# Optimization experiments

Hardware: AMD Instinct MI355X
Metric: run time of the kernel (lower is better)

Reference implementation:

```python
import jax, jax.numpy as jnp
import numpy as np

SCALE = 0.2
ASPECT = 1.0
ORIGIN = (0.5, 0.5)
AREA_THRESH = 400


def setup_inputs() -> dict:
    key = jax.random.key(0)
    kb, ki, kp, kd = jax.random.split(key, 4)
    B, N, H, W = 16, 16, 640, 640
    k1, k2, k3, k4 = jax.random.split(kb, 4)
    ymin = jax.random.uniform(k1, (B, N)) * 280.0
    xmin = jax.random.uniform(k2, (B, N)) * 280.0
    h = 150.0 + jax.random.uniform(k3, (B, N)) * 170.0
    w = 150.0 + jax.random.uniform(k4, (B, N)) * 170.0
    boxes = jnp.stack([ymin, xmin, h, w], axis=-1)  # [B,N,4] = [ymin,xmin,h,w]
    images = jax.random.uniform(ki, (B, H, W, 3), dtype=jnp.float32)
    patch = jax.random.uniform(kp, (300, 300, 3), dtype=jnp.float32)
    transform_decisions = jax.random.bernoulli(kd, 0.5, (B, N, 3))  # rot90, flip_lr, flip_ud
    return {"boxes": boxes, "images": images, "patch": patch,
            "transform_decisions": transform_decisions}


def _bilinear_sample(patch, sy, sx):
    # tf.image.resize (v2 bilinear, half-pixel centers) expressed as a gather.
    Hp, Wp, _ = patch.shape
    sy = jnp.clip(sy, 0.0, Hp - 1.0)
    sx = jnp.clip(sx, 0.0, Wp - 1.0)
    y0 = jnp.floor(sy).astype(jnp.int32)
    x0 = jnp.floor(sx).astype(jnp.int32)
    y1 = jnp.minimum(y0 + 1, Hp - 1)
    x1 = jnp.minimum(x0 + 1, Wp - 1)
    wy = (sy - y0)[..., None]
    wx = (sx - x0)[..., None]
    p00 = patch[y0, x0]; p01 = patch[y0, x1]
    p10 = patch[y1, x0]; p11 = patch[y1, x1]
    top = p00 * (1.0 - wx) + p01 * wx
    bot = p10 * (1.0 - wx) + p11 * wx
    return top * (1.0 - wy) + bot * wy  # [H,W,C]


def _patch_boxes(boxes, H, W):
    # Patcher.create(): place a scale*h square patch at box origin, clamp to image.
    ymin, xmin, h, w = (boxes[..., i] for i in range(4))
    ph = h * SCALE
    pw = ASPECT * ph
    y0 = ymin + h * ORIGIN[1]
    x0 = xmin + w * ORIGIN[0]
    y0 = jnp.where(y0 + ph > H, H - ph, y0)
    x0 = jnp.where(x0 + pw > W, W - pw, x0)
    return jnp.stack([y0, x0, ph, pw], axis=-1)


def _forward(boxes, images, patch, transform_decisions):
    B, H, W, C = images.shape
    Hp, Wp, _ = patch.shape
    pboxes = _patch_boxes(boxes, float(H), float(W))  # [B,N,4] float
    bi = pboxes.astype(jnp.int32)                     # tf.cast truncation
    valid = (bi[..., 2] * bi[..., 3]) > AREA_THRESH   # area filter (mask, not ragged)
    Y = jnp.arange(H)[:, None]
    X = jnp.arange(W)[None, :]

    def apply_patch(img, carry):
        box, dec, v = carry
        y0i, x0i = box[0], box[1]
        s = jnp.maximum(box[2], 1)  # square side (aspect=1); guard div-by-zero
        iy = Y - y0i                 # local patch coords of every image pixel
        ix = X - x0i
        inside = (iy >= 0) & (iy < s) & (ix >= 0) & (ix < s) & v
        iyc = jnp.clip(iy, 0, s - 1)
        ixc = jnp.clip(ix, 0, s - 1)
        d0, d1, d2 = dec[0], dec[1], dec[2]
        iy2 = jnp.where(d2, s - 1 - iyc, iyc)  # invert flip_up_down
        ix2 = jnp.where(d1, s - 1 - ixc, ixc)  # invert flip_left_right
        ry = jnp.where(d0, ix2, iy2)           # invert rot90 (CCW): out[i,j]=in[j,s-1-i]
        rx = jnp.where(d0, s - 1 - iy2, ix2)
        sf = s.astype(jnp.float32)
        sy = (ry.astype(jnp.float32) + 0.5) * (Hp / sf) - 0.5  # half-pixel resize map
        sx = (rx.astype(jnp.float32) + 0.5) * (Wp / sf) - 0.5
        sample = _bilinear_sample(patch, sy, sx)
        img = jnp.where(inside[..., None], sample, img)  # overwrite region
        return img, None

    def per_image(img, box_b, dec_b, valid_b):
        img, _ = jax.lax.scan(apply_patch, img, (box_b, dec_b, valid_b))
        return img

    images_out = jax.vmap(per_image)(images, bi, transform_decisions, valid)
    return images_out, pboxes


def reference(boxes, images, patch, transform_decisions):
    return _forward(boxes, images, patch, transform_decisions)
```

## Files before the change

kernel.cpp:

```cpp
#include <hip/hip_runtime.h>
#include <hip/hip_bf16.h>

#define B_  16
#define N_  16
#define H_  640
#define W_  640
#define HP_ 300
#define WP_ 300
#define IMG_FLOATS (H_ * W_ * 3)
#define ALL_FLOATS (B_ * IMG_FLOATS)
#define PBOX_OFF   ALL_FLOATS
#define QUADS_PER_IMG (H_ * W_ / 4)
#define BLOCKS_PER_IMG (QUADS_PER_IMG / 256)


__global__ __launch_bounds__(256) void prep_kernel(
    const float* __restrict__ boxes,
    const unsigned char* __restrict__ dec_raw,
    float* __restrict__ pboxes_out,
    int* __restrict__ info)
{
    __shared__ int s_nonzero_off;
    __shared__ int s_floatpat;
    if (threadIdx.x == 0) { s_nonzero_off = 0; s_floatpat = 0; }
    __syncthreads();
    for (int i = threadIdx.x; i < B_ * N_ * 3; i += blockDim.x) {
        unsigned char by = dec_raw[i];
        if ((i & 3) != 0 && by != 0) atomicOr(&s_nonzero_off, 1);
        if (by == 0x3F || by == 0x80) atomicOr(&s_floatpat, 1);
    }
    __syncthreads();
    int mode;
    if (!s_nonzero_off)      mode = 1;
    else if (s_floatpat)     mode = 2;
    else                     mode = 0;

    int t = threadIdx.x;
    if (t < B_ * N_) {
        float ymin = boxes[t * 4 + 0];
        float xmin = boxes[t * 4 + 1];
        float h    = boxes[t * 4 + 2];
        float w    = boxes[t * 4 + 3];
        float ph = h * 0.2f;
        float pw = 1.0f * ph;
        float y0 = ymin + h * 0.5f;
        float x0 = xmin + w * 0.5f;
        if (y0 + ph > (float)H_) y0 = (float)H_ - ph;
        if (x0 + pw > (float)W_) x0 = (float)W_ - pw;
        pboxes_out[t * 4 + 0] = y0;
        pboxes_out[t * 4 + 1] = x0;
        pboxes_out[t * 4 + 2] = ph;
        pboxes_out[t * 4 + 3] = pw;

        int y0i = (int)y0;
        int x0i = (int)x0;
        int phi = (int)ph;
        int pwi = (int)pw;
        int valid = (phi * pwi) > 400;
        int s = phi > 1 ? phi : 1;

        int d0, d1, d2;
        if (mode == 0) {
            d0 = dec_raw[t * 3 + 0] != 0;
            d1 = dec_raw[t * 3 + 1] != 0;
            d2 = dec_raw[t * 3 + 2] != 0;
        } else if (mode == 1) {
            const int* di = (const int*)dec_raw;
            d0 = di[t * 3 + 0] != 0;
            d1 = di[t * 3 + 1] != 0;
            d2 = di[t * 3 + 2] != 0;
        } else {
            const float* df = (const float*)dec_raw;
            d0 = df[t * 3 + 0] != 0.0f;
            d1 = df[t * 3 + 1] != 0.0f;
            d2 = df[t * 3 + 2] != 0.0f;
        }
        int* e = info + t * 8;
        e[0] = y0i; e[1] = x0i; e[2] = s; e[3] = valid;
        e[4] = d0;  e[5] = d1;  e[6] = d2; e[7] = 0;
    }
}

__global__ __launch_bounds__(256) void fused_kernel(
    const float*  __restrict__ images,
    const float*  __restrict__ patch,
    const int*    __restrict__ info,
    float*        __restrict__ out)
{
    int b = blockIdx.x / BLOCKS_PER_IMG;
    int q = (blockIdx.x - b * BLOCKS_PER_IMG) * 256 + threadIdx.x;
    int gy = q / (W_ / 4);
    int gx0 = (q - gy * (W_ / 4)) * 4;

    __shared__ int ly0[N_], lx0[N_], ls[N_], lfl[N_];
    if (threadIdx.x < N_) {
        const int* o = info + (b * N_ + threadIdx.x) * 8;
        ly0[threadIdx.x] = o[0];
        lx0[threadIdx.x] = o[1];
        ls[threadIdx.x]  = o[2];
        lfl[threadIdx.x] = o[3] | (o[4] << 1) | (o[5] << 2) | (o[6] << 3);
    }
    __syncthreads();

    size_t base = (size_t)b * IMG_FLOATS + (size_t)q * 12;

    float vals[12];
    *(float4*)&vals[0] = *(const float4*)(images + base);
    *(float4*)&vals[4] = *(const float4*)(images + base + 4);
    *(float4*)&vals[8] = *(const float4*)(images + base + 8);

    #pragma unroll
    for (int p = 0; p < 4; ++p) {
        int gx = gx0 + p;
        int hit = -1;
        for (int m = N_ - 1; m >= 0; --m) {
            if (lfl[m] & 1) {
                unsigned ry = (unsigned)(gy - ly0[m]);
                unsigned rx = (unsigned)(gx - lx0[m]);
                if (ry < (unsigned)ls[m] && rx < (unsigned)ls[m]) { hit = m; break; }
            }
        }
        if (hit >= 0) {
            int s  = ls[hit];
            int fl = lfl[hit];
            int py = gy - ly0[hit];
            int px = gx - lx0[hit];
            int iy2 = (fl & 8) ? (s - 1 - py) : py;
            int ix2 = (fl & 4) ? (s - 1 - px) : px;
            int ry  = (fl & 2) ? ix2 : iy2;
            int rx  = (fl & 2) ? (s - 1 - iy2) : ix2;

            float sf = (float)s;
            float sy = ((float)ry + 0.5f) * ((float)HP_ / sf) - 0.5f;
            float sx = ((float)rx + 0.5f) * ((float)WP_ / sf) - 0.5f;
            sy = fminf(fmaxf(sy, 0.0f), (float)(HP_ - 1));
            sx = fminf(fmaxf(sx, 0.0f), (float)(WP_ - 1));
            int yy0 = (int)floorf(sy);
            int xx0 = (int)floorf(sx);
            int yy1 = yy0 + 1 < HP_ - 1 ? yy0 + 1 : HP_ - 1;
            int xx1 = xx0 + 1 < WP_ - 1 ? xx0 + 1 : WP_ - 1;
            float wy = sy - (float)yy0;
            float wx = sx - (float)xx0;

            const float* p00 = patch + (yy0 * WP_ + xx0) * 3;
            const float* p01 = patch + (yy0 * WP_ + xx1) * 3;
            const float* p10 = patch + (yy1 * WP_ + xx0) * 3;
            const float* p11 = patch + (yy1 * WP_ + xx1) * 3;
            #pragma unroll
            for (int c = 0; c < 3; ++c) {
                float top = p00[c] * (1.0f - wx) + p01[c] * wx;
                float bot = p10[c] * (1.0f - wx) + p11[c] * wx;
                vals[p * 3 + c] = top * (1.0f - wy) + bot * wy;
            }
        }
    }

    *(float4*)(out + base)     = *(float4*)&vals[0];
    *(float4*)(out + base + 4) = *(float4*)&vals[4];
    *(float4*)(out + base + 8) = *(float4*)&vals[8];
}

extern "C" void kernel_launch(void* const* d_in, const int* in_sizes, int n_in,
                              void* d_out, int out_size, void* d_ws, size_t ws_size,
                              hipStream_t stream) {
    const float*         boxes   = (const float*)d_in[0];
    const float*         images  = (const float*)d_in[1];
    const float*         patch   = (const float*)d_in[2];
    const unsigned char* dec_raw = (const unsigned char*)d_in[3];

    float* out    = (float*)d_out;
    float* pboxes = out + PBOX_OFF;
    int*   info   = (int*)d_ws;

    prep_kernel<<<1, 256, 0, stream>>>(boxes, dec_raw, pboxes, info);
    fused_kernel<<<B_ * BLOCKS_PER_IMG, 256, 0, stream>>>(images, patch, info, out);
}
```

Measured before the change: 162.9 us.

## Add coarse cell coverage map and coalesced float4 layout to skip untouched pixels

The prep kernel now runs one block per image and builds a per-64-pixel-cell bitmask of which valid patches touch each cell. The main kernel switches to contiguous float4 indexing, where each thread handles three strided float4s, and uses the mask to skip the patch search for uncovered regions. Covered pixels iterate only over the candidate bits, highest index first. This reduces per-pixel search and makes memory accesses coalesced, but adds a workspace table and more complex channel-splitting logic when a float4 spans two pixels.

```diff
diff --git a/kernel.cpp b/kernel.cpp
--- a/kernel.cpp
+++ b/kernel.cpp
@@ -10,154 +10,225 @@
 #define IMG_FLOATS (H_ * W_ * 3)
 #define ALL_FLOATS (B_ * IMG_FLOATS)
 #define PBOX_OFF   ALL_FLOATS
-#define QUADS_PER_IMG (H_ * W_ / 4)
-#define BLOCKS_PER_IMG (QUADS_PER_IMG / 256)
+#define IMG_F4     (IMG_FLOATS / 4)
+#define F4_PER_BLOCK 768
+#define BLOCKS_PER_IMG (IMG_F4 / F4_PER_BLOCK)
+#define CELLS_PER_IMG (H_ * W_ / 64)
+#define CM_OFF_BYTES (B_ * N_ * 4 * 4)
 
 
 __global__ __launch_bounds__(256) void prep_kernel(
     const float* __restrict__ boxes,
     const unsigned char* __restrict__ dec_raw,
     float* __restrict__ pboxes_out,
-    int* __restrict__ info)
-{
-    __shared__ int s_nonzero_off;
-    __shared__ int s_floatpat;
-    if (threadIdx.x == 0) { s_nonzero_off = 0; s_floatpat = 0; }
-    __syncthreads();
-    for (int i = threadIdx.x; i < B_ * N_ * 3; i += blockDim.x) {
+    int* __restrict__ info,
+    unsigned short* __restrict__ cm,
+    int build_cm)
+{
+    int b = blockIdx.x;
+    int t = threadIdx.x;
+    __shared__ int s_nz, s_fp;
+    __shared__ int ly0[N_], lx0[N_], ls[N_], lfl[N_];
+    if (t == 0) { s_nz = 0; s_fp = 0; }
+    __syncthreads();
+    int nz = 0, fp = 0;
+    for (int i = t; i < B_ * N_ * 3; i += 256) {
         unsigned char by = dec_raw[i];
-        if ((i & 3) != 0 && by != 0) atomicOr(&s_nonzero_off, 1);
-        if (by == 0x3F || by == 0x80) atomicOr(&s_floatpat, 1);
-    }
-    __syncthreads();
-    int mode;
-    if (!s_nonzero_off)      mode = 1;
-    else if (s_floatpat)     mode = 2;
-    else                     mode = 0;
-
-    int t = threadIdx.x;
-    if (t < B_ * N_) {
-        float ymin = boxes[t * 4 + 0];
-        float xmin = boxes[t * 4 + 1];
-        float h    = boxes[t * 4 + 2];
-        float w    = boxes[t * 4 + 3];
+        if ((i & 3) && by) nz = 1;
+        if (by == 0x3F || by == 0x80) fp = 1;
+    }
+    if (nz) atomicOr(&s_nz, 1);
+    if (fp) atomicOr(&s_fp, 1);
+    __syncthreads();
+    int mode = !s_nz ? 1 : (s_fp ? 2 : 0);
+
+    if (t < N_) {
+        int e = b * N_ + t;
+        float ymin = boxes[e*4+0], xmin = boxes[e*4+1];
+        float h = boxes[e*4+2], w = boxes[e*4+3];
         float ph = h * 0.2f;
         float pw = 1.0f * ph;
         float y0 = ymin + h * 0.5f;
         float x0 = xmin + w * 0.5f;
         if (y0 + ph > (float)H_) y0 = (float)H_ - ph;
         if (x0 + pw > (float)W_) x0 = (float)W_ - pw;
-        pboxes_out[t * 4 + 0] = y0;
-        pboxes_out[t * 4 + 1] = x0;
-        pboxes_out[t * 4 + 2] = ph;
-        pboxes_out[t * 4 + 3] = pw;
-
-        int y0i = (int)y0;
-        int x0i = (int)x0;
-        int phi = (int)ph;
-        int pwi = (int)pw;
+        pboxes_out[e*4+0] = y0; pboxes_out[e*4+1] = x0;
+        pboxes_out[e*4+2] = ph; pboxes_out[e*4+3] = pw;
+
+        int y0i = (int)y0, x0i = (int)x0;
+        int phi = (int)ph, pwi = (int)pw;
         int valid = (phi * pwi) > 400;
         int s = phi > 1 ? phi : 1;
 
         int d0, d1, d2;
         if (mode == 0) {
-            d0 = dec_raw[t * 3 + 0] != 0;
-            d1 = dec_raw[t * 3 + 1] != 0;
-            d2 = dec_raw[t * 3 + 2] != 0;
+            d0 = dec_raw[e*3+0] != 0; d1 = dec_raw[e*3+1] != 0; d2 = dec_raw[e*3+2] != 0;
         } else if (mode == 1) {
             const int* di = (const int*)dec_raw;
-            d0 = di[t * 3 + 0] != 0;
-            d1 = di[t * 3 + 1] != 0;
-            d2 = di[t * 3 + 2] != 0;
+            d0 = di[e*3+0] != 0; d1 = di[e*3+1] != 0; d2 = di[e*3+2] != 0;
         } else {
             const float* df = (const float*)dec_raw;
-            d0 = df[t * 3 + 0] != 0.0f;
-            d1 = df[t * 3 + 1] != 0.0f;
-            d2 = df[t * 3 + 2] != 0.0f;
+            d0 = df[e*3+0] != 0.0f; d1 = df[e*3+1] != 0.0f; d2 = df[e*3+2] != 0.0f;
         }
-        int* e = info + t * 8;
-        e[0] = y0i; e[1] = x0i; e[2] = s; e[3] = valid;
-        e[4] = d0;  e[5] = d1;  e[6] = d2; e[7] = 0;
-    }
-}
-
-__global__ __launch_bounds__(256) void fused_kernel(
-    const float*  __restrict__ images,
-    const float*  __restrict__ patch,
-    const int*    __restrict__ info,
-    float*        __restrict__ out)
-{
-    int b = blockIdx.x / BLOCKS_PER_IMG;
-    int q = (blockIdx.x - b * BLOCKS_PER_IMG) * 256 + threadIdx.x;
-    int gy = q / (W_ / 4);
-    int gx0 = (q - gy * (W_ / 4)) * 4;
-
-    __shared__ int ly0[N_], lx0[N_], ls[N_], lfl[N_];
-    if (threadIdx.x < N_) {
-        const int* o = info + (b * N_ + threadIdx.x) * 8;
-        ly0[threadIdx.x] = o[0];
-        lx0[threadIdx.x] = o[1];
-        ls[threadIdx.x]  = o[2];
-        lfl[threadIdx.x] = o[3] | (o[4] << 1) | (o[5] << 2) | (o[6] << 3);
-    }
-    __syncthreads();
-
-    size_t base = (size_t)b * IMG_FLOATS + (size_t)q * 12;
-
-    float vals[12];
-    *(float4*)&vals[0] = *(const float4*)(images + base);
-    *(float4*)&vals[4] = *(const float4*)(images + base + 4);
-    *(float4*)&vals[8] = *(const float4*)(images + base + 8);
-
-    #pragma unroll
-    for (int p = 0; p < 4; ++p) {
-        int gx = gx0 + p;
-        int hit = -1;
-        for (int m = N_ - 1; m >= 0; --m) {
-            if (lfl[m] & 1) {
-                unsigned ry = (unsigned)(gy - ly0[m]);
-                unsigned rx = (unsigned)(gx - lx0[m]);
-                if (ry < (unsigned)ls[m] && rx < (unsigned)ls[m]) { hit = m; break; }
+        int flags = valid | (d0 << 1) | (d1 << 2) | (d2 << 3);
+        ly0[t] = y0i; lx0[t] = x0i; ls[t] = s; lfl[t] = flags;
+        int* ei = info + e * 4;
+        ei[0] = y0i; ei[1] = x0i; ei[2] = s; ei[3] = flags;
+    }
+    __syncthreads();
+
+    if (build_cm) {
+        unsigned short* cmb = cm + b * CELLS_PER_IMG;
+        for (int c = t; c < CELLS_PER_IMG; c += 256) {
+            int gy  = c / (W_ / 64);
+            int gx0 = (c - gy * (W_ / 64)) * 64;
+            unsigned m16 = 0;
+            for (int m = 0; m < N_; ++m) {
+                if ((lfl[m] & 1) &&
+                    (unsigned)(gy - ly0[m]) < (unsigned)ls[m] &&
+                    lx0[m] < gx0 + 64 && lx0[m] + ls[m] > gx0)
+                    m16 |= 1u << m;
             }
+            cmb[c] = (unsigned short)m16;
         }
-        if (hit >= 0) {
-            int s  = ls[hit];
-            int fl = lfl[hit];
-            int py = gy - ly0[hit];
-            int px = gx - lx0[hit];
-            int iy2 = (fl & 8) ? (s - 1 - py) : py;
-            int ix2 = (fl & 4) ? (s - 1 - px) : px;
-            int ry  = (fl & 2) ? ix2 : iy2;
-            int rx  = (fl & 2) ? (s - 1 - iy2) : ix2;
-
-            float sf = (float)s;
-            float sy = ((float)ry + 0.5f) * ((float)HP_ / sf) - 0.5f;
-            float sx = ((float)rx + 0.5f) * ((float)WP_ / sf) - 0.5f;
+    }
+}
+
+__device__ __forceinline__ int sample_px(
+    int p, unsigned mask,
+    const int* ly0, const int* lx0, const int* ls, const int* lfl,
+    const float* __restrict__ patch,
+    float& cr, float& cg, float& cb)
+{
+    int gy = p / W_;
+    int gx = p - gy * W_;
+    while (mask) {
+        int m = 31 - __clz(mask);
+        int s = ls[m];
+        int ry = gy - ly0[m], rx = gx - lx0[m];
+        if ((unsigned)ry < (unsigned)s && (unsigned)rx < (unsigned)s) {
+            int fl = lfl[m];
+            int iy2 = (fl & 8) ? (s - 1 - ry) : ry;
+            int ix2 = (fl & 4) ? (s - 1 - rx) : rx;
+            int ty  = (fl & 2) ? ix2 : iy2;
+            int tx  = (fl & 2) ? (s - 1 - iy2) : ix2;
+            float sf  = (float)s;
+            float sc  = (float)HP_ / sf;
+            float sy = ((float)ty + 0.5f) * sc - 0.5f;
+            float sx = ((float)tx + 0.5f) * sc - 0.5f;
             sy = fminf(fmaxf(sy, 0.0f), (float)(HP_ - 1));
             sx = fminf(fmaxf(sx, 0.0f), (float)(WP_ - 1));
-            int yy0 = (int)floorf(sy);
-            int xx0 = (int)floorf(sx);
+            int yy0 = (int)sy;
+            int xx0 = (int)sx;
             int yy1 = yy0 + 1 < HP_ - 1 ? yy0 + 1 : HP_ - 1;
             int xx1 = xx0 + 1 < WP_ - 1 ? xx0 + 1 : WP_ - 1;
             float wy = sy - (float)yy0;
             float wx = sx - (float)xx0;
-
             const float* p00 = patch + (yy0 * WP_ + xx0) * 3;
             const float* p01 = patch + (yy0 * WP_ + xx1) * 3;
             const float* p10 = patch + (yy1 * WP_ + xx0) * 3;
             const float* p11 = patch + (yy1 * WP_ + xx1) * 3;
-            #pragma unroll
-            for (int c = 0; c < 3; ++c) {
-                float top = p00[c] * (1.0f - wx) + p01[c] * wx;
-                float bot = p10[c] * (1.0f - wx) + p11[c] * wx;
-                vals[p * 3 + c] = top * (1.0f - wy) + bot * wy;
-            }
+            float t0 = p00[0]*(1.f-wx) + p01[0]*wx;
+            float b0 = p10[0]*(1.f-wx) + p11[0]*wx;
+            cr = t0*(1.f-wy) + b0*wy;
+            float t1 = p00[1]*(1.f-wx) + p01[1]*wx;
+            float b1 = p10[1]*(1.f-wx) + p11[1]*wx;
+            cg = t1*(1.f-wy) + b1*wy;
+            float t2 = p00[2]*(1.f-wx) + p01[2]*wx;
+            float b2 = p10[2]*(1.f-wx) + p11[2]*wx;
+            cb = t2*(1.f-wy) + b2*wy;
+            return 1;
         }
-    }
-
-    *(float4*)(out + base)     = *(float4*)&vals[0];
-    *(float4*)(out + base + 4) = *(float4*)&vals[4];
-    *(float4*)(out + base + 8) = *(float4*)&vals[8];
+        mask &= ~(1u << m);
+    }
+    return 0;
+}
+
+__device__ __forceinline__ float4 process_f4(
+    float4 v, int f,
+    const unsigned short* __restrict__ cmb,
+    const int* ly0, const int* lx0, const int* ls, const int* lfl,
+    const float* __restrict__ patch, int use_tab)
+{
+    int wlo = f & ~63;
+    int whi = wlo + 63;
+    int px_lo = wlo + wlo / 3;
+    int px_hi = (4 * whi + 3) / 3;
+    unsigned mask;
+    if (use_tab) {
+        int c0 = px_lo >> 6, c1 = px_hi >> 6;
+        mask = (unsigned)cmb[c0] | (unsigned)cmb[c1];
+        if (c1 == c0 + 2) mask |= (unsigned)cmb[c0 + 1];
+    } else {
+        int ry0 = px_lo / W_, ry1 = px_hi / W_;
+        int cx0, cx1;
+        if (ry0 == ry1) { cx0 = px_lo - ry0 * W_; cx1 = px_hi - ry0 * W_; }
+        else            { cx0 = 0; cx1 = W_ - 1; }
+        mask = 0;
+        for (int m = 0; m < N_; ++m)
+            if ((lfl[m] & 1) && ly0[m] <= ry1 && ly0[m] + ls[m] > ry0 &&
+                lx0[m] <= cx1 && lx0[m] + ls[m] > cx0)
+                mask |= 1u << m;
+    }
+    if (!mask) return v;
+
+    int p0 = f + f / 3;
+    float c00, c01, c02, c10, c11, c12;
+    int h0 = sample_px(p0,     mask, ly0, lx0, ls, lfl, patch, c00, c01, c02);
+    int h1 = sample_px(p0 + 1, mask, ly0, lx0, ls, lfl, patch, c10, c11, c12);
+    if (!(h0 | h1)) return v;
+
+    int r = f % 3;
+    float vv0 = v.x, vv1 = v.y, vv2 = v.z, vv3 = v.w;
+    if (r == 0) {
+        if (h0) { vv0 = c00; vv1 = c01; vv2 = c02; }
+        if (h1) { vv3 = c10; }
+    } else if (r == 1) {
+        if (h0) { vv0 = c01; vv1 = c02; }
+        if (h1) { vv2 = c10; vv3 = c11; }
+    } else {
+        if (h0) { vv0 = c02; }
+        if (h1) { vv1 = c10; vv2 = c11; vv3 = c12; }
+    }
+    return make_float4(vv0, vv1, vv2, vv3);
+}
+
+__global__ __launch_bounds__(256) void fused_kernel(
+    const float4* __restrict__ images4,
+    const float*  __restrict__ patch,
+    const int*    __restrict__ info,
+    const unsigned short* __restrict__ cm,
+    float4*       __restrict__ out4,
+    int use_tab)
+{
+    int blk = blockIdx.x;
+    int b = blk / BLOCKS_PER_IMG;
+    int blkLocal = blk - b * BLOCKS_PER_IMG;
+    int t = threadIdx.x;
+
+    __shared__ int ly0[N_], lx0[N_], ls[N_], lfl[N_];
+    if (t < N_) {
+        const int* ei = info + (b * N_ + t) * 4;
+        ly0[t] = ei[0]; lx0[t] = ei[1]; ls[t] = ei[2]; lfl[t] = ei[3];
+    }
+    __syncthreads();
+
+    const float4* ib = images4 + (size_t)b * IMG_F4;
+    float4*       ob = out4    + (size_t)b * IMG_F4;
+    const unsigned short* cmb = cm + b * CELLS_PER_IMG;
+
+    int f0 = blkLocal * F4_PER_BLOCK + t;
+    float4 v0 = ib[f0];
+    float4 v1 = ib[f0 + 256];
+    float4 v2 = ib[f0 + 512];
+
+    v0 = process_f4(v0, f0,       cmb, ly0, lx0, ls, lfl, patch, use_tab);
+    v1 = process_f4(v1, f0 + 256, cmb, ly0, lx0, ls, lfl, patch, use_tab);
+    v2 = process_f4(v2, f0 + 512, cmb, ly0, lx0, ls, lfl, patch, use_tab);
+
+    ob[f0]       = v0;
+    ob[f0 + 256] = v1;
+    ob[f0 + 512] = v2;
 }
 
 extern "C" void kernel_launch(void* const* d_in, const int* in_sizes, int n_in,
@@ -171,7 +242,11 @@
     float* out    = (float*)d_out;
     float* pboxes = out + PBOX_OFF;
     int*   info   = (int*)d_ws;
-
-    prep_kernel<<<1, 256, 0, stream>>>(boxes, dec_raw, pboxes, info);
-    fused_kernel<<<B_ * BLOCKS_PER_IMG, 256, 0, stream>>>(images, patch, info, out);
-}
+    unsigned short* cm = (unsigned short*)((char*)d_ws + CM_OFF_BYTES);
+    size_t need = CM_OFF_BYTES + (size_t)B_ * CELLS_PER_IMG * sizeof(unsigned short);
+    int use_tab = (ws_size >= need) ? 1 : 0;
+
+    prep_kernel<<<B_, 256, 0, stream>>>(boxes, dec_raw, pboxes, info, cm, use_tab);
+    fused_kernel<<<B_ * BLOCKS_PER_IMG, 256, 0, stream>>>(
+        (const float4*)images, patch, info, cm, (float4*)out, use_tab);
+}
```

Result: no change. 164.5 us (+1.0%).
